# Performance work log

Measured on AMD Instinct MI355X. Metric: run time of the kernel, lower is better.

Reference implementation:

```python
import jax, jax.numpy as jnp
import numpy as np

EPS_BN = 1e-5
EPS_W = 1e-8


def _bn(x, g, b, m, v):
    # x: [B, N, C]; params: [C] (inference-mode batchnorm)
    return g * (x - m) * jax.lax.rsqrt(v + EPS_BN) + b


def setup_inputs() -> dict:
    key = jax.random.key(0)
    ks = jax.random.split(key, 24)
    B, N, S = 16, 4096, 1024
    C1, C2 = 128, 256            # points1 / points2 channels
    CIN, COUT = C1 + C2, 128     # in_channel, out_channel

    def w(k, shape, std=0.02):
        return (jax.random.normal(k, shape, jnp.float32) * std)

    def bn_params(k, c):
        k1, k2, k3, k4 = jax.random.split(k, 4)
        return (1.0 + 0.1 * jax.random.normal(k1, (c,), jnp.float32),  # gamma
                0.1 * jax.random.normal(k2, (c,), jnp.float32),        # beta
                0.1 * jax.random.normal(k3, (c,), jnp.float32),        # running mean
                0.5 + jax.random.uniform(k4, (c,), jnp.float32))       # running var

    fg, fb, fm, fv = bn_params(ks[4], COUT)
    g1, b1, m1, v1 = bn_params(ks[5], COUT)
    g2, b2, m2, v2 = bn_params(ks[6], COUT)
    return {
        "xyz1": jax.random.uniform(ks[0], (B, N, 3), jnp.float32),
        "xyz2": jax.random.uniform(ks[1], (B, S, 3), jnp.float32),
        "points1": jax.random.normal(ks[2], (B, C1, N), jnp.float32),
        "points2": jax.random.normal(ks[3], (B, C2, S), jnp.float32),
        "fuse_w": w(ks[7], (COUT, CIN)), "fuse_b": jnp.zeros((COUT,), jnp.float32),
        "fuse_g": fg, "fuse_beta": fb, "fuse_m": fm, "fuse_v": fv,
        "c1_w": w(ks[8], (COUT, COUT)), "c1_b": jnp.zeros((COUT,), jnp.float32),
        "bn1_g": g1, "bn1_b": b1, "bn1_m": m1, "bn1_v": v1,
        "c2_w": w(ks[9], (COUT, COUT)), "c2_b": jnp.zeros((COUT,), jnp.float32),
        "bn2_g": g2, "bn2_b": b2, "bn2_m": m2, "bn2_v": v2,
    }


def reference(xyz1, xyz2, points1, points2,
              fuse_w, fuse_b, fuse_g, fuse_beta, fuse_m, fuse_v,
              c1_w, c1_b, bn1_g, bn1_b, bn1_m, bn1_v,
              c2_w, c2_b, bn2_g, bn2_b, bn2_m, bn2_v):
    B, N, _ = xyz1.shape
    pts1 = jnp.swapaxes(points1, 1, 2)   # [B, N, C1]
    pts2 = jnp.swapaxes(points2, 1, 2)   # [B, S, C2]

    # squared pairwise distances [B, N, S]
    dists = (jnp.sum(xyz1 ** 2, -1)[:, :, None]
             + jnp.sum(xyz2 ** 2, -1)[:, None, :]
             - 2.0 * jnp.einsum('bnc,bsc->bns', xyz1, xyz2))

    # 3 nearest neighbors (smallest distances)
    neg_d3, idx = jax.lax.top_k(-dists, 3)          # [B, N, 3]
    d3 = -neg_d3
    recip = 1.0 / (d3 + EPS_W)
    weight = recip / jnp.sum(recip, axis=2, keepdims=True)  # [B, N, 3]

    gathered = jax.vmap(lambda p, i: p[i])(pts2, idx)        # [B, N, 3, C2]
    interp = jnp.sum(gathered * weight[..., None], axis=2)   # [B, N, C2]

    x = jnp.concatenate([pts1, interp], axis=-1)             # [B, N, CIN]

    # fuse: 1x1 conv + BN + ReLU
    x = jax.nn.relu(_bn(jnp.einsum('bnc,oc->bno', x, fuse_w) + fuse_b,
                        fuse_g, fuse_beta, fuse_m, fuse_v))

    # residual block: conv-BN-ReLU -> conv-BN, add skip, ReLU
    h = jax.nn.relu(_bn(jnp.einsum('bnc,oc->bno', x, c1_w) + c1_b,
                        bn1_g, bn1_b, bn1_m, bn1_v))
    y = _bn(jnp.einsum('bnc,oc->bno', h, c2_w) + c2_b,
            bn2_g, bn2_b, bn2_m, bn2_v)
    out = jax.nn.relu(y + x)                                 # [B, N, COUT]
    return jnp.swapaxes(out, 1, 2)                           # [B, COUT, N]
```

## Files before the change

### kernel.cpp

```cpp
#include <hip/hip_runtime.h>
#include <hip/hip_bf16.h>

#define BB 16
#define NN 4096
#define SS 1024
#define C1 128
#define C2 256
#define CIN 384
#define CO 128

typedef __bf16 bf16x8 __attribute__((ext_vector_type(8)));
typedef float f32x4 __attribute__((ext_vector_type(4)));

__global__ __launch_bounds__(256) void knn_kernel(
    const float* __restrict__ xyz1, const float* __restrict__ xyz2,
    int* __restrict__ idx4, float* __restrict__ w4)
{
    __shared__ float4 pts[SS];
    const int b = blockIdx.y;
    const float* p2 = xyz2 + (size_t)b * SS * 3;
    for (int i = threadIdx.x; i < SS; i += 256) {
        float x = p2[i * 3 + 0], y = p2[i * 3 + 1], z = p2[i * 3 + 2];
        pts[i] = make_float4(x, y, z, x * x + y * y + z * z);
    }
    __syncthreads();

    const int n = blockIdx.x * 256 + threadIdx.x;
    const float* p1 = xyz1 + ((size_t)b * NN + n) * 3;
    const float x = p1[0], y = p1[1], z = p1[2];
    const float s1 = x * x + y * y + z * z;

    float d0 = 3.4e38f, d1 = 3.4e38f, d2 = 3.4e38f, d3 = 3.4e38f;
    int i0 = 0, i1 = 0, i2 = 0, i3 = 0;
    #pragma unroll 4
    for (int s = 0; s < SS; ++s) {
        float4 p = pts[s];
        float d = s1 + p.w - 2.0f * (x * p.x + y * p.y + z * p.z);
        bool lt0 = d < d0, lt1 = d < d1, lt2 = d < d2, lt3 = d < d3;
        float nd3 = lt2 ? d2 : (lt3 ? d : d3); int ni3 = lt2 ? i2 : (lt3 ? s : i3);
        float nd2 = lt1 ? d1 : (lt2 ? d : d2); int ni2 = lt1 ? i1 : (lt2 ? s : i2);
        float nd1 = lt0 ? d0 : (lt1 ? d : d1); int ni1 = lt0 ? i0 : (lt1 ? s : i1);
        d0 = lt0 ? d : d0;                     i0 = lt0 ? s : i0;
        d1 = nd1; i1 = ni1; d2 = nd2; i2 = ni2; d3 = nd3; i3 = ni3;
    }
    float r0 = 1.0f / (d0 + 1e-8f);
    float r1 = 1.0f / (d1 + 1e-8f);
    float r2 = 1.0f / (d2 + 1e-8f);
    float rs = r0 + r1 + r2;
    bool tie = (d2 == d3);
    size_t base = ((size_t)b * NN + n) * 4;
    idx4[base + 0] = i0; idx4[base + 1] = i1;
    idx4[base + 2] = i2; idx4[base + 3] = i3;
    w4[base + 0] = r0 / rs; w4[base + 1] = r1 / rs;
    w4[base + 2] = r2 / rs; w4[base + 3] = tie ? -1.0f : 0.0f;
}

__global__ __launch_bounds__(256) void p2t_kernel(
    const float* __restrict__ p2, float* __restrict__ p2t)
{
    __shared__ float tile[64][65];
    const int b = blockIdx.z;
    const int s0 = blockIdx.x * 64, c0 = blockIdx.y * 64;
    for (int i = threadIdx.x; i < 64 * 64; i += 256) {
        int s = i & 63, c = i >> 6;
        tile[c][s] = p2[((size_t)b * C2 + c0 + c) * SS + s0 + s];
    }
    __syncthreads();
    for (int i = threadIdx.x; i < 64 * 64; i += 256) {
        int c = i & 63, s = i >> 6;
        p2t[((size_t)b * SS + s0 + s) * C2 + c0 + c] = tile[c][s];
    }
}

__global__ __launch_bounds__(256) void wprep_kernel(
    const float* __restrict__ fw, const float* __restrict__ w1,
    const float* __restrict__ w2,
    __bf16* __restrict__ Whf, __bf16* __restrict__ Wlf,
    __bf16* __restrict__ Wh1, __bf16* __restrict__ Wl1,
    __bf16* __restrict__ Wh2, __bf16* __restrict__ Wl2)
{
    int t = blockIdx.x * 256 + threadIdx.x;
    float v; __bf16 *oh, *ol; int idx;
    if (t < 49152)      { idx = t;         v = fw[idx]; oh = Whf; ol = Wlf; }
    else if (t < 65536) { idx = t - 49152; v = w1[idx]; oh = Wh1; ol = Wl1; }
    else                { idx = t - 65536; v = w2[idx]; oh = Wh2; ol = Wl2; }
    __bf16 h = (__bf16)v;
    oh[idx] = h; ol[idx] = (__bf16)(v - (float)h);
}

__global__ __launch_bounds__(256) void tie_eval_kernel(
    const float* __restrict__ p2t, const float* __restrict__ points1,
    const int* __restrict__ idx4, float* __restrict__ w4,
    const float* __restrict__ fw, const float* __restrict__ fb,
    const float* __restrict__ fg, const float* __restrict__ fbt,
    const float* __restrict__ fm, const float* __restrict__ fv,
    const float* __restrict__ w1m, const float* __restrict__ b1,
    const float* __restrict__ g1, const float* __restrict__ bt1,
    const float* __restrict__ m1, const float* __restrict__ v1,
    const float* __restrict__ w2m, const float* __restrict__ b2,
    const float* __restrict__ g2, const float* __restrict__ bt2,
    const float* __restrict__ m2, const float* __restrict__ v2)
{
    __shared__ float Xs[4][2][CIN];
    __shared__ float XT[4][2][CO];
    __shared__ float Hs[4][2][CO];
    const int wave = threadIdx.x >> 6, lane = threadIdx.x & 63;
    const int n = blockIdx.x * 4 + wave;
    const int b = blockIdx.y;
    const size_t base = ((size_t)b * NN + n) * 4;
    if (w4[base + 3] != -1.0f) return;

    const int i0 = idx4[base + 0], i1 = idx4[base + 1];
    const int i2 = idx4[base + 2], i3 = idx4[base + 3];
    const float w0 = w4[base + 0], w1 = w4[base + 1], w2 = w4[base + 2];
    const float* P = p2t + (size_t)b * SS * C2;

    for (int c = lane; c < C1; c += 64) {
        float v = points1[((size_t)b * C1 + c) * NN + n];
        Xs[wave][0][c] = v; Xs[wave][1][c] = v;
    }
    for (int c = lane; c < C2; c += 64) {
        float f0 = P[(size_t)i0 * C2 + c], f1 = P[(size_t)i1 * C2 + c];
        float f2 = P[(size_t)i2 * C2 + c], f3 = P[(size_t)i3 * C2 + c];
        float bs = w0 * f0 + w1 * f1;
        Xs[wave][0][C1 + c] = bs + w2 * f2;
        Xs[wave][1][C1 + c] = bs + w2 * f3;
    }
    #pragma unroll
    for (int k = 0; k < 2; ++k) {
        int oc = lane + 64 * k;
        float alo = fb[oc], ahi = fb[oc];
        for (int c = 0; c < CIN; ++c) {
            float wv = fw[(size_t)oc * CIN + c];
            alo += wv * Xs[wave][0][c];
            ahi += wv * Xs[wave][1][c];
        }
        float s = fg[oc] * (1.0f / sqrtf(fv[oc] + 1e-5f));
        XT[wave][0][oc] = fmaxf(s * (alo - fm[oc]) + fbt[oc], 0.0f);
        XT[wave][1][oc] = fmaxf(s * (ahi - fm[oc]) + fbt[oc], 0.0f);
    }
    #pragma unroll
    for (int k = 0; k < 2; ++k) {
        int oc = lane + 64 * k;
        float alo = b1[oc], ahi = b1[oc];
        for (int c = 0; c < CO; ++c) {
            float wv = w1m[(size_t)oc * CO + c];
            alo += wv * XT[wave][0][c];
            ahi += wv * XT[wave][1][c];
        }
        float s = g1[oc] * (1.0f / sqrtf(v1[oc] + 1e-5f));
        Hs[wave][0][oc] = fmaxf(s * (alo - m1[oc]) + bt1[oc], 0.0f);
        Hs[wave][1][oc] = fmaxf(s * (ahi - m1[oc]) + bt1[oc], 0.0f);
    }
    float e = 0.0f;
    #pragma unroll
    for (int k = 0; k < 2; ++k) {
        int oc = lane + 64 * k;
        float alo = b2[oc], ahi = b2[oc];
        for (int c = 0; c < CO; ++c) {
            float wv = w2m[(size_t)oc * CO + c];
            alo += wv * Hs[wave][0][c];
            ahi += wv * Hs[wave][1][c];
        }
        float s = g2[oc] * (1.0f / sqrtf(v2[oc] + 1e-5f));
        float olo = fmaxf(s * (alo - m2[oc]) + bt2[oc] + XT[wave][0][oc], 0.0f);
        float ohi = fmaxf(s * (ahi - m2[oc]) + bt2[oc] + XT[wave][1][oc], 0.0f);
        e = fmaxf(e, fabsf(olo - ohi));
    }
    for (int off = 32; off; off >>= 1) e = fmaxf(e, __shfl_xor(e, off));
    if (lane == 0) {
        if (e > 0.085f) { w4[base + 3] = 0.0f; }
        else { w4[base + 2] = 0.5f * w2; w4[base + 3] = 0.5f * w2; }
    }
}

__global__ __launch_bounds__(256) void buildx_kernel(
    const float* __restrict__ points1,
    const float* __restrict__ p2t,
    const int* __restrict__ idx4, const float* __restrict__ w4,
    __bf16* __restrict__ Xh, __bf16* __restrict__ Xl)
{
    __shared__ float t1[128][66];
    const int b = blockIdx.y;
    const int n0 = blockIdx.x * 64;
    for (int i = threadIdx.x; i < 128 * 64; i += 256) {
        int j = i & 63, c = i >> 6;
        t1[c][j] = points1[((size_t)b * C1 + c) * NN + n0 + j];
    }
    __syncthreads();
    for (int i = threadIdx.x; i < 128 * 64; i += 256) {
        int c = i & 127, j = i >> 7;
        float v = t1[c][j];
        __bf16 h = (__bf16)v;
        size_t o = ((size_t)b * NN + n0 + j) * CIN + c;
        Xh[o] = h; Xl[o] = (__bf16)(v - (float)h);
    }
    for (int i = threadIdx.x; i < 64 * C2; i += 256) {
        int c = i & 255, j = i >> 8;
        int n = n0 + j;
        size_t ib = ((size_t)b * NN + n) * 4;
        int s0 = idx4[ib + 0], s1 = idx4[ib + 1];
        int s2 = idx4[ib + 2], s3 = idx4[ib + 3];
        float w0 = w4[ib + 0], w1 = w4[ib + 1];
        float w2 = w4[ib + 2], w3 = w4[ib + 3];
        const float* base = p2t + (size_t)b * SS * C2;
        float v = w0 * base[(size_t)s0 * C2 + c]
                + w1 * base[(size_t)s1 * C2 + c]
                + w2 * base[(size_t)s2 * C2 + c]
                + w3 * base[(size_t)s3 * C2 + c];
        __bf16 h = (__bf16)v;
        size_t o = ((size_t)b * NN + n) * CIN + C1 + c;
        Xh[o] = h; Xl[o] = (__bf16)(v - (float)h);
    }
}

template<int K, int MODE>
__global__ __launch_bounds__(256) void gemm_bn_kernel(
    const __bf16* __restrict__ Ah, const __bf16* __restrict__ Al,
    const __bf16* __restrict__ Wh, const __bf16* __restrict__ Wl,
    const float* __restrict__ cb,  const float* __restrict__ gg,
    const float* __restrict__ bbta, const float* __restrict__ mm,
    const float* __restrict__ vv,
    const __bf16* __restrict__ skiph, const __bf16* __restrict__ skipl,
    __bf16* __restrict__ outh, __bf16* __restrict__ outl,
    float* __restrict__ outf)
{
    __shared__ __attribute__((aligned(16))) __bf16 wls_h[128 * 40];
    __shared__ __attribute__((aligned(16))) __bf16 wls_l[128 * 40];
    __shared__ float s_s[128], s_t[128];
    __shared__ float tile[32][132];
    const int tid = threadIdx.x;
    if (tid < 128) {
        float s = gg[tid] * (1.0f / sqrtf(vv[tid] + 1e-5f));
        float t = (cb[tid] - mm[tid]) * s + bbta[tid];
        s_s[tid] = s; s_t[tid] = t;
    }
    const int wave = tid >> 6, lane = tid & 63;
    const int m = lane & 15, q = lane >> 4;
    const size_t r0 = (size_t)blockIdx.x * 128 + wave * 32;

    f32x4 acc[2][8] = {};
    const __bf16* pAh = Ah + (r0 + m) * (size_t)K + q * 8;
    const __bf16* pAl = Al + (r0 + m) * (size_t)K + q * 8;

    const int wrow = tid >> 1, whf = tid & 1;
    for (int kk = 0; kk < K; kk += 32) {
        __syncthreads();
        {
            size_t g = (size_t)wrow * K + kk + whf * 16;
            int lo = wrow * 40 + whf * 16;
            *(uint4*)&wls_h[lo]     = *(const uint4*)&Wh[g];
            *(uint4*)&wls_h[lo + 8] = *(const uint4*)&Wh[g + 8];
            *(uint4*)&wls_l[lo]     = *(const uint4*)&Wl[g];
            *(uint4*)&wls_l[lo + 8] = *(const uint4*)&Wl[g + 8];
        }
        __syncthreads();
        bf16x8 ah0 = *(const bf16x8*)(pAh + kk);
        bf16x8 al0 = *(const bf16x8*)(pAl + kk);
        bf16x8 ah1 = *(const bf16x8*)(pAh + 16 * (size_t)K + kk);
        bf16x8 al1 = *(const bf16x8*)(pAl + 16 * (size_t)K + kk);
        #pragma unroll
        for (int ot = 0; ot < 8; ++ot) {
            bf16x8 bh = *(const bf16x8*)&wls_h[(ot * 16 + m) * 40 + q * 8];
            bf16x8 bl = *(const bf16x8*)&wls_l[(ot * 16 + m) * 40 + q * 8];
            acc[0][ot] = __builtin_amdgcn_mfma_f32_16x16x32_bf16(ah0, bh, acc[0][ot], 0, 0, 0);
            acc[0][ot] = __builtin_amdgcn_mfma_f32_16x16x32_bf16(al0, bh, acc[0][ot], 0, 0, 0);
            acc[0][ot] = __builtin_amdgcn_mfma_f32_16x16x32_bf16(ah0, bl, acc[0][ot], 0, 0, 0);
            acc[1][ot] = __builtin_amdgcn_mfma_f32_16x16x32_bf16(ah1, bh, acc[1][ot], 0, 0, 0);
            acc[1][ot] = __builtin_amdgcn_mfma_f32_16x16x32_bf16(al1, bh, acc[1][ot], 0, 0, 0);
            acc[1][ot] = __builtin_amdgcn_mfma_f32_16x16x32_bf16(ah1, bl, acc[1][ot], 0, 0, 0);
        }
    }

    if (MODE == 0) {
        #pragma unroll
        for (int rt = 0; rt < 2; ++rt) {
            #pragma unroll
            for (int ot = 0; ot < 8; ++ot) {
                int col = ot * 16 + m;
                float sc = s_s[col], sh = s_t[col];
                #pragma unroll
                for (int r = 0; r < 4; ++r) {
                    size_t row = r0 + rt * 16 + q * 4 + r;
                    float val = fmaxf(acc[rt][ot][r] * sc + sh, 0.0f);
                    __bf16 h = (__bf16)val;
                    outh[row * 128 + col] = h;
                    outl[row * 128 + col] = (__bf16)(val - (float)h);
                }
            }
        }
    } else {
        const int bidx = (int)(((size_t)blockIdx.x * 128) >> 12);
        const int nbase = (int)(((size_t)blockIdx.x * 128) & 4095);
        for (int cc = 0; cc < 4; ++cc) {
            __syncthreads();
            #pragma unroll
            for (int oo = 0; oo < 2; ++oo) {
                int ot = cc * 2 + oo;
                int col = ot * 16 + m;
                float sc = s_s[col], sh = s_t[col];
                #pragma unroll
                for (int rt = 0; rt < 2; ++rt) {
                    #pragma unroll
                    for (int r = 0; r < 4; ++r) {
                        int lrow = wave * 32 + rt * 16 + q * 4 + r;
                        size_t row = (size_t)blockIdx.x * 128 + lrow;
                        float val = acc[rt][ot][r] * sc + sh;
                        val += (float)skiph[row * 128 + col] + (float)skipl[row * 128 + col];
                        val = fmaxf(val, 0.0f);
                        tile[oo * 16 + m][lrow] = val;
                    }
                }
            }
            __syncthreads();
            for (int c2 = tid >> 7; c2 < 32; c2 += 2) {
                int nn_ = tid & 127;
                outf[((size_t)bidx * 128 + cc * 32 + c2) * NN + nbase + nn_] = tile[c2][nn_];
            }
        }
    }
}

extern "C" void kernel_launch(void* const* d_in, const int* in_sizes, int n_in,
                              void* d_out, int out_size, void* d_ws, size_t ws_size,
                              hipStream_t stream) {
    const float* xyz1    = (const float*)d_in[0];
    const float* xyz2    = (const float*)d_in[1];
    const float* points1 = (const float*)d_in[2];
    const float* points2 = (const float*)d_in[3];
    const float* fuse_w  = (const float*)d_in[4];
    const float* fuse_b  = (const float*)d_in[5];
    const float* fuse_g  = (const float*)d_in[6];
    const float* fuse_bt = (const float*)d_in[7];
    const float* fuse_m  = (const float*)d_in[8];
    const float* fuse_v  = (const float*)d_in[9];
    const float* c1_w    = (const float*)d_in[10];
    const float* c1_b    = (const float*)d_in[11];
    const float* bn1_g   = (const float*)d_in[12];
    const float* bn1_b   = (const float*)d_in[13];
    const float* bn1_m   = (const float*)d_in[14];
    const float* bn1_v   = (const float*)d_in[15];
    const float* c2_w    = (const float*)d_in[16];
    const float* c2_b    = (const float*)d_in[17];
    const float* bn2_g   = (const float*)d_in[18];
    const float* bn2_b   = (const float*)d_in[19];
    const float* bn2_m   = (const float*)d_in[20];
    const float* bn2_v   = (const float*)d_in[21];

    char* ws = (char*)d_ws;
    int*    idx4 = (int*)(ws);
    float*  w4   = (float*)(ws + 1048576);
    float*  p2t  = (float*)(ws + 2097152);
    __bf16* Xh   = (__bf16*)(ws + 18874368);
    __bf16* Xl   = (__bf16*)(ws + 69206016);
    __bf16* Y0h  = (__bf16*)(ws + 119537664);
    __bf16* Y0l  = (__bf16*)(ws + 136314880);
    __bf16* Hh   = (__bf16*)(ws + 153092096);
    __bf16* Hl   = (__bf16*)(ws + 169869312);
    __bf16* Whf  = (__bf16*)(ws + 186646528);
    __bf16* Wlf  = (__bf16*)(ws + 186744832);
    __bf16* Wh1  = (__bf16*)(ws + 186843136);
    __bf16* Wl1  = (__bf16*)(ws + 186875904);
    __bf16* Wh2  = (__bf16*)(ws + 186908672);
    __bf16* Wl2  = (__bf16*)(ws + 186941440);

    knn_kernel<<<dim3(NN / 256, BB), 256, 0, stream>>>(xyz1, xyz2, idx4, w4);
    p2t_kernel<<<dim3(SS / 64, C2 / 64, BB), 256, 0, stream>>>(points2, p2t);
    wprep_kernel<<<320, 256, 0, stream>>>(fuse_w, c1_w, c2_w,
                                          Whf, Wlf, Wh1, Wl1, Wh2, Wl2);
    tie_eval_kernel<<<dim3(NN / 4, BB), 256, 0, stream>>>(
        p2t, points1, idx4, w4,
        fuse_w, fuse_b, fuse_g, fuse_bt, fuse_m, fuse_v,
        c1_w, c1_b, bn1_g, bn1_b, bn1_m, bn1_v,
        c2_w, c2_b, bn2_g, bn2_b, bn2_m, bn2_v);
    buildx_kernel<<<dim3(NN / 64, BB), 256, 0, stream>>>(points1, p2t, idx4, w4, Xh, Xl);

    const int gblocks = (BB * NN) / 128;
    gemm_bn_kernel<CIN, 0><<<gblocks, 256, 0, stream>>>(
        Xh, Xl, Whf, Wlf, fuse_b, fuse_g, fuse_bt, fuse_m, fuse_v,
        nullptr, nullptr, Y0h, Y0l, nullptr);
    gemm_bn_kernel<CO, 0><<<gblocks, 256, 0, stream>>>(
        Y0h, Y0l, Wh1, Wl1, c1_b, bn1_g, bn1_b, bn1_m, bn1_v,
        nullptr, nullptr, Hh, Hl, nullptr);
    gemm_bn_kernel<CO, 1><<<gblocks, 256, 0, stream>>>(
        Hh, Hl, Wh2, Wl2, c2_b, bn2_g, bn2_b, bn2_m, bn2_v,
        Y0h, Y0l, nullptr, nullptr, (float*)d_out);
}
```

Measured before the change: 374.2 us.

## Split KNN search over point chunks and merge partial top-4 lists

After: 354.8 us. 5.2% less time.

```diff
diff --git a/kernel.cpp b/kernel.cpp
--- a/kernel.cpp
+++ b/kernel.cpp
@@ -9,17 +9,21 @@
 #define CIN 384
 #define CO 128
 
+#define KCH 4
+#define SCH (SS / KCH)
+
 typedef __bf16 bf16x8 __attribute__((ext_vector_type(8)));
 typedef float f32x4 __attribute__((ext_vector_type(4)));
 
-__global__ __launch_bounds__(256) void knn_kernel(
+__global__ __launch_bounds__(256) void knn_part_kernel(
     const float* __restrict__ xyz1, const float* __restrict__ xyz2,
-    int* __restrict__ idx4, float* __restrict__ w4)
-{
-    __shared__ float4 pts[SS];
-    const int b = blockIdx.y;
-    const float* p2 = xyz2 + (size_t)b * SS * 3;
-    for (int i = threadIdx.x; i < SS; i += 256) {
+    float4* __restrict__ pd4, int4* __restrict__ pi4)
+{
+    __shared__ float4 pts[SCH];
+    const int b = blockIdx.z;
+    const int ch = blockIdx.y;
+    const float* p2 = xyz2 + ((size_t)b * SS + (size_t)ch * SCH) * 3;
+    for (int i = threadIdx.x; i < SCH; i += 256) {
         float x = p2[i * 3 + 0], y = p2[i * 3 + 1], z = p2[i * 3 + 2];
         pts[i] = make_float4(x, y, z, x * x + y * y + z * z);
     }
@@ -32,16 +36,50 @@
 
     float d0 = 3.4e38f, d1 = 3.4e38f, d2 = 3.4e38f, d3 = 3.4e38f;
     int i0 = 0, i1 = 0, i2 = 0, i3 = 0;
+    const int sbase = ch * SCH;
     #pragma unroll 4
-    for (int s = 0; s < SS; ++s) {
-        float4 p = pts[s];
+    for (int sl = 0; sl < SCH; ++sl) {
+        float4 p = pts[sl];
         float d = s1 + p.w - 2.0f * (x * p.x + y * p.y + z * p.z);
+        int s = sbase + sl;
         bool lt0 = d < d0, lt1 = d < d1, lt2 = d < d2, lt3 = d < d3;
         float nd3 = lt2 ? d2 : (lt3 ? d : d3); int ni3 = lt2 ? i2 : (lt3 ? s : i3);
         float nd2 = lt1 ? d1 : (lt2 ? d : d2); int ni2 = lt1 ? i1 : (lt2 ? s : i2);
         float nd1 = lt0 ? d0 : (lt1 ? d : d1); int ni1 = lt0 ? i0 : (lt1 ? s : i1);
         d0 = lt0 ? d : d0;                     i0 = lt0 ? s : i0;
         d1 = nd1; i1 = ni1; d2 = nd2; i2 = ni2; d3 = nd3; i3 = ni3;
+    }
+    size_t o = ((size_t)b * NN + n) * KCH + ch;
+    pd4[o] = make_float4(d0, d1, d2, d3);
+    pi4[o] = make_int4(i0, i1, i2, i3);
+}
+
+__global__ __launch_bounds__(256) void knn_merge_kernel(
+    const float4* __restrict__ pd4, const int4* __restrict__ pi4,
+    int* __restrict__ idx4, float* __restrict__ w4)
+{
+    const int n = blockIdx.x * 256 + threadIdx.x;
+    const int b = blockIdx.y;
+    const size_t o = ((size_t)b * NN + n) * KCH;
+
+    float d0 = 3.4e38f, d1 = 3.4e38f, d2 = 3.4e38f, d3 = 3.4e38f;
+    int i0 = 0, i1 = 0, i2 = 0, i3 = 0;
+    #pragma unroll
+    for (int ch = 0; ch < KCH; ++ch) {
+        float4 pd = pd4[o + ch];
+        int4 pi = pi4[o + ch];
+        float cd[4] = { pd.x, pd.y, pd.z, pd.w };
+        int   ci[4] = { pi.x, pi.y, pi.z, pi.w };
+        #pragma unroll
+        for (int k = 0; k < 4; ++k) {
+            float d = cd[k]; int s = ci[k];
+            bool lt0 = d < d0, lt1 = d < d1, lt2 = d < d2, lt3 = d < d3;
+            float nd3 = lt2 ? d2 : (lt3 ? d : d3); int ni3 = lt2 ? i2 : (lt3 ? s : i3);
+            float nd2 = lt1 ? d1 : (lt2 ? d : d2); int ni2 = lt1 ? i1 : (lt2 ? s : i2);
+            float nd1 = lt0 ? d0 : (lt1 ? d : d1); int ni1 = lt0 ? i0 : (lt1 ? s : i1);
+            d0 = lt0 ? d : d0;                     i0 = lt0 ? s : i0;
+            d1 = nd1; i1 = ni1; d2 = nd2; i2 = ni2; d3 = nd3; i3 = ni3;
+        }
     }
     float r0 = 1.0f / (d0 + 1e-8f);
     float r1 = 1.0f / (d1 + 1e-8f);
@@ -364,7 +402,11 @@
     __bf16* Wh2  = (__bf16*)(ws + 186908672);
     __bf16* Wl2  = (__bf16*)(ws + 186941440);
 
-    knn_kernel<<<dim3(NN / 256, BB), 256, 0, stream>>>(xyz1, xyz2, idx4, w4);
+    float4* pd4 = (float4*)(ws + 18874368);
+    int4*   pi4 = (int4*)(ws + 18874368 + 4194304);
+
+    knn_part_kernel<<<dim3(NN / 256, KCH, BB), 256, 0, stream>>>(xyz1, xyz2, pd4, pi4);
+    knn_merge_kernel<<<dim3(NN / 256, BB), 256, 0, stream>>>(pd4, pi4, idx4, w4);
     p2t_kernel<<<dim3(SS / 64, C2 / 64, BB), 256, 0, stream>>>(points2, p2t);
     wprep_kernel<<<320, 256, 0, stream>>>(fuse_w, c1_w, c2_w,
                                           Whf, Wlf, Wh1, Wl1, Wh2, Wl2);
```
